# Kernel optimization log

Hardware: AMD Instinct MI355X
Metric: run time of the kernel (lower is better)

## Reference

```python
import jax, jax.numpy as jnp
import numpy as np

B, S, DA, DV, DU, L, M = 16, 256, 1, 32, 1, 4, 12


def conv1x1(x, w, b):
    # x: [B,C,H,W], w: [O,C], b: [O]
    return jnp.einsum('bchw,oc->bohw', x, w) + b[None, :, None, None]


def setup_inputs() -> dict:
    key = jax.random.key(0)
    ks = jax.random.split(key, 12)
    sc = 0.02
    return {
        'x':    jax.random.normal(ks[0], (B, S, S, DA), dtype=jnp.float32),
        'p_w':  sc * jax.random.normal(ks[1], (DV, DA + 2), dtype=jnp.float32),
        'p_b':  sc * jax.random.normal(ks[2], (DV,), dtype=jnp.float32),
        'ws_w': sc * jax.random.normal(ks[3], (L, DV, DV), dtype=jnp.float32),
        'ws_b': sc * jax.random.normal(ks[4], (L, DV), dtype=jnp.float32),
        'w1r':  sc * jax.random.normal(ks[5], (L, DV, DV, M, M), dtype=jnp.float32),
        'w1i':  sc * jax.random.normal(ks[6], (L, DV, DV, M, M), dtype=jnp.float32),
        'w2r':  sc * jax.random.normal(ks[7], (L, DV, DV, M, M), dtype=jnp.float32),
        'w2i':  sc * jax.random.normal(ks[8], (L, DV, DV, M, M), dtype=jnp.float32),
        'q_w':  sc * jax.random.normal(ks[9], (DU, DV), dtype=jnp.float32),
        'q_b':  sc * jax.random.normal(ks[10], (DU,), dtype=jnp.float32),
    }


def fourier_layer(x, w1r, w1i, w2r, w2i):
    # x: [B,C,H,W]; FFT norm None == 'backward' (numpy/jax default)
    b, c, h, w = x.shape
    x_ft = jnp.fft.rfft2(x)                       # [B,C,H,W//2+1] complex
    W1 = w1r + 1j * w1i                           # [C,C,M,M]
    W2 = w2r + 1j * w2i
    top = jnp.einsum('bixy,ioxy->boxy', x_ft[:, :, :M, :M], W1)
    bot = jnp.einsum('bixy,ioxy->boxy', x_ft[:, :, -M:, :M], W2)
    out_ft = jnp.zeros((b, c, h, w // 2 + 1), dtype=x_ft.dtype)
    out_ft = out_ft.at[:, :, :M, :M].set(top)
    out_ft = out_ft.at[:, :, h - M:, :M].set(bot)
    return jnp.fft.irfft2(out_ft, s=(h, w))


def reference(x, p_w, p_b, ws_w, ws_b, w1r, w1i, w2r, w2i, q_w, q_b):
    b, sx, sy, _ = x.shape
    # grid as in get_grid (requires sx == sy, as the original implicitly does)
    gx = jnp.linspace(-1.0, 1.0, sx, dtype=jnp.float32)
    gy = jnp.linspace(-1.0, 1.0, sy, dtype=jnp.float32)
    gridx = jnp.broadcast_to(gx.reshape(1, 1, sx, 1), (b, sy, sx, 1))
    gridy = jnp.broadcast_to(gy.reshape(1, sy, 1, 1), (b, sy, sx, 1))
    grid = jnp.concatenate([gridy, gridx], axis=-1)     # [B,Sy,Sx,2]
    h = jnp.concatenate([x, grid], axis=-1)             # [B,S,S,DA+2]
    h = jnp.transpose(h, (0, 3, 1, 2))                  # NCHW
    h = conv1x1(h, p_w, p_b)                            # lifting
    for i in range(L):
        x1 = fourier_layer(h, w1r[i], w1i[i], w2r[i], w2i[i])
        x2 = conv1x1(h, ws_w[i], ws_b[i])
        h = x1 + x2
        if i < L - 1:
            h = jax.nn.relu(h)
    h = conv1x1(h, q_w, q_b)                            # projection -> [B,1,S,S]
    return jnp.transpose(h, (0, 2, 3, 1)).squeeze(-1)   # [B,S,S]
```

## Files before the change

kernel.cpp:

```cpp
#include <hip/hip_runtime.h>
#include <math.h>

#define NB 16
#define SS 256
#define DV 32
#define MM 12
#define MK 24
#define LL 4
#define TWO_PI_N 0.024543692606170259679f


__global__ __launch_bounds__(256) void k_prep(const float* __restrict__ ws_w,
        float* __restrict__ twT, float* __restrict__ wT)
{
    int j = threadIdx.x;
    #pragma unroll
    for (int k = 0; k < MM; ++k) {
        float ang = TWO_PI_N * (float)((k * j) & 255);
        float s, c; sincosf(ang, &s, &c);
        twT[j * (MM * 2) + 2 * k]     = c;
        twT[j * (MM * 2) + 2 * k + 1] = -s;
    }
    for (int idx = threadIdx.x; idx < LL * DV * DV; idx += 256) {
        int l = idx >> 10, rem = idx & 1023, co = rem >> 5, ci = rem & 31;
        wT[(l * DV + ci) * DV + co] = ws_w[(l * DV + co) * DV + ci];
    }
}

__global__ __launch_bounds__(256) void k_lift(const float* __restrict__ x,
        const float* __restrict__ p_w, const float* __restrict__ p_b,
        float* __restrict__ h)
{
    int tid = threadIdx.x;
    int lane = tid & 63;
    int w = __builtin_amdgcn_readfirstlane(tid >> 6);
    int b  = blockIdx.x >> 6;
    int iy = ((blockIdx.x & 63) << 2) + w;
    int j0 = lane << 2;

    float4 xv = *(const float4*)(x + ((size_t)(b * SS + iy)) * SS + j0);
    float gy = -1.f + 2.f * (float)iy * (1.f / 255.f);
    float4 gx;
    gx.x = -1.f + 2.f * (float)j0 * (1.f / 255.f);
    gx.y = gx.x + 2.f / 255.f; gx.z = gx.y + 2.f / 255.f; gx.w = gx.z + 2.f / 255.f;

    float* hb = h + ((size_t)b * DV * SS + iy) * SS + j0;
    #pragma unroll
    for (int c = 0; c < DV; ++c) {
        float w0 = p_w[3*c], w1 = p_w[3*c+1], w2 = p_w[3*c+2], bb = p_b[c];
        float4 v;
        v.x = w0 * xv.x + w1 * gy + w2 * gx.x + bb;
        v.y = w0 * xv.y + w1 * gy + w2 * gx.y + bb;
        v.z = w0 * xv.z + w1 * gy + w2 * gx.z + bb;
        v.w = w0 * xv.w + w1 * gy + w2 * gx.w + bb;
        *(float4*)(hb + (size_t)c * SS * SS) = v;
    }
}

__global__ __launch_bounds__(512, 4) void k_rowdft(const float* __restrict__ h,
        const float* __restrict__ twT, float* __restrict__ A)
{
    __shared__ float red[MM * 2][SS];
    int tid = threadIdx.x;
    int iy = tid & 255;
    int half = __builtin_amdgcn_readfirstlane(tid >> 8);
    int b = blockIdx.x >> 5, c = blockIdx.x & 31;

    const float4* hr = (const float4*)(h + ((size_t)blockIdx.x * SS + iy) * SS
                                         + half * 128);
    float ar[MM], ai[MM];
    #pragma unroll
    for (int k = 0; k < MM; ++k) { ar[k] = 0.f; ai[k] = 0.f; }

    #pragma unroll 4
    for (int j4 = 0; j4 < 32; ++j4) {
        float4 v = hr[j4];
        float vv[4] = {v.x, v.y, v.z, v.w};
        #pragma unroll
        for (int u = 0; u < 4; ++u) {
            const float* twj = twT + (size_t)(half * 128 + 4 * j4 + u) * (MM * 2);
            float vu = vv[u];
            #pragma unroll
            for (int k = 0; k < 6; ++k) {
                ar[2*k]   += vu * twj[4*k];
                ai[2*k]   += vu * twj[4*k + 1];
                ar[2*k+1] += vu * twj[4*k + 2];
                ai[2*k+1] += vu * twj[4*k + 3];
            }
        }
    }

    if (half == 0) {
        #pragma unroll
        for (int k = 0; k < MM; ++k) {
            red[2*k][iy]     = ar[k];
            red[2*k + 1][iy] = ai[k];
        }
    }
    __syncthreads();
    if (half == 1) {
        #pragma unroll
        for (int ky = 0; ky < MM; ++ky) {
            float2 val;
            val.x = ar[ky] + red[2*ky][iy];
            val.y = ai[ky] + red[2*ky + 1][iy];
            size_t o = ((((size_t)b * MM + ky) * DV + c) * SS + iy) * 2;
            *(float2*)&A[o] = val;
        }
    }
}

__global__ __launch_bounds__(256, 4) void k_coldft(const float* __restrict__ A,
        float* __restrict__ Fin)
{
    int blk = blockIdx.x;
    int mg = blk & 3;
    int bk = blk >> 2;
    int tid = threadIdx.x;
    int c = tid >> 3, ch = tid & 7;
    int iy0 = ch * 32;

    const float2* Ap = (const float2*)(A + ((size_t)bk * DV + c) * SS * 2);

    float fr[6], fi[6], pc[6], ps[6], sc[6], ssn[6];
    #pragma unroll
    for (int k = 0; k < 6; ++k) {
        int m = mg * 6 + k;
        int f = (m < MM) ? m : (232 + m);
        float s, cc;
        sincosf(TWO_PI_N * (float)f, &s, &cc);
        sc[k] = cc; ssn[k] = s;
        sincosf(TWO_PI_N * (float)((f * iy0) & 255), &s, &cc);
        pc[k] = cc; ps[k] = s;
        fr[k] = fi[k] = 0.f;
    }
    #pragma unroll 4
    for (int i = 0; i < 32; ++i) {
        float2 a = Ap[iy0 + i];
        #pragma unroll
        for (int k = 0; k < 6; ++k) {
            fr[k] += a.x * pc[k] + a.y * ps[k];
            fi[k] += a.y * pc[k] - a.x * ps[k];
            float np = pc[k] * sc[k] - ps[k] * ssn[k];
            float nq = pc[k] * ssn[k] + ps[k] * sc[k];
            pc[k] = np; ps[k] = nq;
        }
    }
    #pragma unroll
    for (int m = 1; m < 8; m <<= 1) {
        #pragma unroll
        for (int k = 0; k < 6; ++k) {
            fr[k] += __shfl_xor(fr[k], m, 64);
            fi[k] += __shfl_xor(fi[k], m, 64);
        }
    }
    #pragma unroll
    for (int k = 0; k < 6; ++k) {
        if (ch == k) {
            int m = mg * 6 + k;
            size_t o = (((size_t)bk * DV + c) * MK + m) * 2;
            Fin[o] = fr[k]; Fin[o + 1] = fi[k];
        }
    }
}

__global__ __launch_bounds__(256) void k_mix2(const float* __restrict__ FinG,
        const float* __restrict__ w1r, const float* __restrict__ w1i,
        const float* __restrict__ w2r, const float* __restrict__ w2i,
        float* __restrict__ F, int l)
{
    __shared__ float Fin[DV][MK * 2 + 2];
    int tid = threadIdx.x;
    int b = blockIdx.x / MM, ky = blockIdx.x % MM;

    const float* Fs = FinG + ((size_t)(b * MM + ky)) * DV * MK * 2;
    for (int idx = tid; idx < DV * MK * 2; idx += 256) {
        int c = idx / (MK * 2), r = idx % (MK * 2);
        Fin[c][r] = Fs[idx];
    }
    __syncthreads();

    int o = tid >> 3, set = tid & 7;
    float scale = ((ky == 0) ? 1.0f : 2.0f) * (1.0f / 65536.0f);
    #pragma unroll
    for (int k = 0; k < 3; ++k) {
        int m = set + 8 * k;
        const float* Wr; const float* Wi; int xm;
        if (m < MM) { Wr = w1r; Wi = w1i; xm = m; }
        else        { Wr = w2r; Wi = w2i; xm = m - MM; }
        float orr = 0.f, oii = 0.f;
        for (int i = 0; i < DV; ++i) {
            float gr = Fin[i][2 * m], gi = Fin[i][2 * m + 1];
            size_t wi = ((size_t)(l * DV + i) * DV + o) * (MM * MM) + xm * MM + ky;
            float wr = Wr[wi], wim = Wi[wi];
            orr += gr * wr - gi * wim;
            oii += gr * wim + gi * wr;
        }
        size_t off = ((((size_t)b * MM + ky) * DV + o) * MK + m) * 2;
        F[off] = orr * scale; F[off + 1] = oii * scale;
    }
}

__global__ __launch_bounds__(384) void k_inv1(const float* __restrict__ F,
        float* __restrict__ g)
{
    __shared__ float itw[MK * 2];
    int tid = threadIdx.x;
    int b = blockIdx.x >> 8, iy = blockIdx.x & 255;
    if (tid < MK) {
        int f = (tid < MM) ? tid : (232 + tid);
        float ang = TWO_PI_N * (float)((f * iy) & 255);
        float s, c; sincosf(ang, &s, &c);
        itw[2 * tid] = c; itw[2 * tid + 1] = s;
    }
    __syncthreads();

    int ky = tid >> 5, co = tid & 31;
    const float2* Fp = (const float2*)(F + ((((size_t)b * MM + ky) * DV + co) * MK) * 2);
    float gr = 0.f, gi = 0.f;
    #pragma unroll
    for (int m = 0; m < MK; ++m) {
        float2 fv = Fp[m];
        float ic = itw[2 * m], is = itw[2 * m + 1];
        gr += fv.x * ic - fv.y * is;
        gi += fv.x * is + fv.y * ic;
    }
    size_t o = (((size_t)(b * SS + iy)) * MM + ky) * (DV * 2) + 2 * co;
    g[o] = gr; g[o + 1] = gi;
}

template<int FINAL>
__global__ __launch_bounds__(256, 2) void k_pt(float* __restrict__ h,
        const float* __restrict__ g, const float* __restrict__ wT,
        const float* __restrict__ ws_b, const float* __restrict__ q_w,
        const float* __restrict__ q_b, float* __restrict__ out, int l)
{
    int tid = threadIdx.x;
    int lane = tid & 63;
    int w = __builtin_amdgcn_readfirstlane(tid >> 6);
    int b  = blockIdx.x >> 6;
    int iy = ((blockIdx.x & 63) << 2) + w;
    int j0 = lane << 2;

    float* hb = h + ((size_t)b * DV * SS + iy) * SS + j0;
    const float* wt  = wT + (size_t)l * DV * DV;
    const float* wsb = ws_b + (size_t)l * DV;

    float4 acc[DV];
    #pragma unroll
    for (int co = 0; co < DV; ++co) {
        float bv = wsb[co];
        acc[co].x = bv; acc[co].y = bv; acc[co].z = bv; acc[co].w = bv;
    }

    #pragma unroll 4
    for (int ci = 0; ci < DV; ++ci) {
        float4 hv = *(const float4*)(hb + (size_t)ci * SS * SS);
        const float* wc = wt + ci * DV;
        #pragma unroll
        for (int co = 0; co < DV; ++co) {
            float wv = wc[co];
            acc[co].x += wv * hv.x; acc[co].y += wv * hv.y;
            acc[co].z += wv * hv.z; acc[co].w += wv * hv.w;
        }
    }

    const float* gp = g + ((size_t)(b * SS + iy)) * (MM * DV * 2);
    #pragma unroll 2
    for (int ky = 0; ky < MM; ++ky) {
        float s0, c0, st, ct;
        sincosf(TWO_PI_N * (float)((ky * j0) & 255), &s0, &c0);
        sincosf(TWO_PI_N * (float)ky, &st, &ct);
        float cs[4], sn[4];
        cs[0] = c0; sn[0] = s0;
        #pragma unroll
        for (int u = 1; u < 4; ++u) {
            float nc = cs[u-1] * ct - sn[u-1] * st;
            float ns = sn[u-1] * ct + cs[u-1] * st;
            cs[u] = nc; sn[u] = ns;
        }
        const float* Gk = gp + ky * (DV * 2);
        #pragma unroll
        for (int co = 0; co < DV; ++co) {
            float gr = Gk[2 * co], gi = Gk[2 * co + 1];
            acc[co].x += gr * cs[0] - gi * sn[0];
            acc[co].y += gr * cs[1] - gi * sn[1];
            acc[co].z += gr * cs[2] - gi * sn[2];
            acc[co].w += gr * cs[3] - gi * sn[3];
        }
    }

    if (FINAL) {
        float qb = q_b[0];
        float4 o4; o4.x = qb; o4.y = qb; o4.z = qb; o4.w = qb;
        #pragma unroll
        for (int co = 0; co < DV; ++co) {
            float qv = q_w[co];
            o4.x += qv * acc[co].x; o4.y += qv * acc[co].y;
            o4.z += qv * acc[co].z; o4.w += qv * acc[co].w;
        }
        *(float4*)(out + ((size_t)(b * SS + iy)) * SS + j0) = o4;
    } else {
        #pragma unroll
        for (int co = 0; co < DV; ++co) {
            float4 v;
            v.x = fmaxf(acc[co].x, 0.f); v.y = fmaxf(acc[co].y, 0.f);
            v.z = fmaxf(acc[co].z, 0.f); v.w = fmaxf(acc[co].w, 0.f);
            *(float4*)(hb + (size_t)co * SS * SS) = v;
        }
    }
}

extern "C" void kernel_launch(void* const* d_in, const int* in_sizes, int n_in,
                              void* d_out, int out_size, void* d_ws, size_t ws_size,
                              hipStream_t stream)
{
    const float* x    = (const float*)d_in[0];
    const float* p_w  = (const float*)d_in[1];
    const float* p_b  = (const float*)d_in[2];
    const float* ws_w = (const float*)d_in[3];
    const float* ws_b = (const float*)d_in[4];
    const float* w1r  = (const float*)d_in[5];
    const float* w1i  = (const float*)d_in[6];
    const float* w2r  = (const float*)d_in[7];
    const float* w2i  = (const float*)d_in[8];
    const float* q_w  = (const float*)d_in[9];
    const float* q_b  = (const float*)d_in[10];
    float* out = (float*)d_out;

    float* h   = (float*)d_ws;
    float* A   = h   + (size_t)NB * DV * SS * SS;
    float* F   = A   + (size_t)NB * MM * DV * SS * 2;
    float* g   = F   + (size_t)NB * MM * DV * MK * 2;
    float* Fin = g   + (size_t)NB * SS * MM * DV * 2;
    float* twT = Fin + (size_t)NB * MM * DV * MK * 2;
    float* wT  = twT + (size_t)SS * MM * 2;

    dim3 blk(256);
    k_prep<<<1, blk, 0, stream>>>(ws_w, twT, wT);
    k_lift<<<NB * 64, blk, 0, stream>>>(x, p_w, p_b, h);
    for (int l = 0; l < LL; ++l) {
        k_rowdft<<<NB * DV, dim3(512), 0, stream>>>(h, twT, A);
        k_coldft<<<NB * MM * 4, blk, 0, stream>>>(A, Fin);
        k_mix2<<<NB * MM, blk, 0, stream>>>(Fin, w1r, w1i, w2r, w2i, F, l);
        k_inv1<<<NB * SS, dim3(384), 0, stream>>>(F, g);
        if (l < LL - 1)
            k_pt<0><<<NB * 64, blk, 0, stream>>>(h, g, wT, ws_b,
                                                 nullptr, nullptr, nullptr, l);
        else
            k_pt<1><<<NB * 64, blk, 0, stream>>>(h, g, wT, ws_b,
                                                 q_w, q_b, out, l);
    }
}
```

Measured before the change: 832.0 us.

## Fuse column DFT with spectral mixing; retile pointwise kernel with precomputed twiddles

```diff
diff --git a/kernel.cpp b/kernel.cpp
--- a/kernel.cpp
+++ b/kernel.cpp
@@ -11,7 +11,7 @@
 
 
 __global__ __launch_bounds__(256) void k_prep(const float* __restrict__ ws_w,
-        float* __restrict__ twT, float* __restrict__ wT)
+        float* __restrict__ twT, float* __restrict__ wT, float* __restrict__ tw2)
 {
     int j = threadIdx.x;
     #pragma unroll
@@ -20,6 +20,8 @@
         float s, c; sincosf(ang, &s, &c);
         twT[j * (MM * 2) + 2 * k]     = c;
         twT[j * (MM * 2) + 2 * k + 1] = -s;
+        tw2[(k * SS + j) * 2]     = c;
+        tw2[(k * SS + j) * 2 + 1] = s;
     }
     for (int idx = threadIdx.x; idx < LL * DV * DV; idx += 256) {
         int l = idx >> 10, rem = idx & 1023, co = rem >> 5, ci = rem & 31;
@@ -110,12 +112,16 @@
     }
 }
 
-__global__ __launch_bounds__(256, 4) void k_coldft(const float* __restrict__ A,
-        float* __restrict__ Fin)
-{
+__global__ __launch_bounds__(256, 4) void k_cm(const float* __restrict__ A,
+        const float* __restrict__ w1r, const float* __restrict__ w1i,
+        const float* __restrict__ w2r, const float* __restrict__ w2i,
+        float* __restrict__ F, int l)
+{
+    __shared__ float FinS[DV][6][2];
     int blk = blockIdx.x;
     int mg = blk & 3;
     int bk = blk >> 2;
+    int ky = bk % MM;
     int tid = threadIdx.x;
     int c = tid >> 3, ch = tid & 7;
     int iy0 = ch * 32;
@@ -156,47 +162,27 @@
     }
     #pragma unroll
     for (int k = 0; k < 6; ++k) {
-        if (ch == k) {
-            int m = mg * 6 + k;
-            size_t o = (((size_t)bk * DV + c) * MK + m) * 2;
-            Fin[o] = fr[k]; Fin[o + 1] = fi[k];
-        }
-    }
-}
-
-__global__ __launch_bounds__(256) void k_mix2(const float* __restrict__ FinG,
-        const float* __restrict__ w1r, const float* __restrict__ w1i,
-        const float* __restrict__ w2r, const float* __restrict__ w2i,
-        float* __restrict__ F, int l)
-{
-    __shared__ float Fin[DV][MK * 2 + 2];
-    int tid = threadIdx.x;
-    int b = blockIdx.x / MM, ky = blockIdx.x % MM;
-
-    const float* Fs = FinG + ((size_t)(b * MM + ky)) * DV * MK * 2;
-    for (int idx = tid; idx < DV * MK * 2; idx += 256) {
-        int c = idx / (MK * 2), r = idx % (MK * 2);
-        Fin[c][r] = Fs[idx];
+        if (ch == k) { FinS[c][k][0] = fr[k]; FinS[c][k][1] = fi[k]; }
     }
     __syncthreads();
 
-    int o = tid >> 3, set = tid & 7;
-    float scale = ((ky == 0) ? 1.0f : 2.0f) * (1.0f / 65536.0f);
-    #pragma unroll
-    for (int k = 0; k < 3; ++k) {
-        int m = set + 8 * k;
+    if (ch < 6) {
+        int o = c;
+        int m = mg * 6 + ch;
         const float* Wr; const float* Wi; int xm;
         if (m < MM) { Wr = w1r; Wi = w1i; xm = m; }
         else        { Wr = w2r; Wi = w2i; xm = m - MM; }
+        float scale = ((ky == 0) ? 1.0f : 2.0f) * (1.0f / 65536.0f);
         float orr = 0.f, oii = 0.f;
+        #pragma unroll 4
         for (int i = 0; i < DV; ++i) {
-            float gr = Fin[i][2 * m], gi = Fin[i][2 * m + 1];
+            float gr = FinS[i][ch][0], gi = FinS[i][ch][1];
             size_t wi = ((size_t)(l * DV + i) * DV + o) * (MM * MM) + xm * MM + ky;
             float wr = Wr[wi], wim = Wi[wi];
             orr += gr * wr - gi * wim;
             oii += gr * wim + gi * wr;
         }
-        size_t off = ((((size_t)b * MM + ky) * DV + o) * MK + m) * 2;
+        size_t off = (((size_t)bk * DV + o) * MK + m) * 2;
         F[off] = orr * scale; F[off + 1] = oii * scale;
     }
 }
@@ -230,83 +216,69 @@
 }
 
 template<int FINAL>
-__global__ __launch_bounds__(256, 2) void k_pt(float* __restrict__ h,
+__global__ __launch_bounds__(256, 4) void k_pt(float* __restrict__ h,
         const float* __restrict__ g, const float* __restrict__ wT,
-        const float* __restrict__ ws_b, const float* __restrict__ q_w,
-        const float* __restrict__ q_b, float* __restrict__ out, int l)
+        const float* __restrict__ ws_b, const float* __restrict__ tw2,
+        const float* __restrict__ q_w, const float* __restrict__ q_b,
+        float* __restrict__ out, int l)
 {
     int tid = threadIdx.x;
     int lane = tid & 63;
     int w = __builtin_amdgcn_readfirstlane(tid >> 6);
-    int b  = blockIdx.x >> 6;
-    int iy = ((blockIdx.x & 63) << 2) + w;
-    int j0 = lane << 2;
+    int b  = blockIdx.x >> 7;
+    int iy = ((blockIdx.x & 127) << 1) + (w >> 1);
+    int j0 = ((w & 1) << 7) + (lane << 1);
 
     float* hb = h + ((size_t)b * DV * SS + iy) * SS + j0;
     const float* wt  = wT + (size_t)l * DV * DV;
     const float* wsb = ws_b + (size_t)l * DV;
 
-    float4 acc[DV];
+    float2 acc[DV];
     #pragma unroll
     for (int co = 0; co < DV; ++co) {
         float bv = wsb[co];
-        acc[co].x = bv; acc[co].y = bv; acc[co].z = bv; acc[co].w = bv;
+        acc[co].x = bv; acc[co].y = bv;
     }
 
     #pragma unroll 4
     for (int ci = 0; ci < DV; ++ci) {
-        float4 hv = *(const float4*)(hb + (size_t)ci * SS * SS);
+        float2 hv = *(const float2*)(hb + (size_t)ci * SS * SS);
         const float* wc = wt + ci * DV;
         #pragma unroll
         for (int co = 0; co < DV; ++co) {
             float wv = wc[co];
             acc[co].x += wv * hv.x; acc[co].y += wv * hv.y;
-            acc[co].z += wv * hv.z; acc[co].w += wv * hv.w;
         }
     }
 
     const float* gp = g + ((size_t)(b * SS + iy)) * (MM * DV * 2);
     #pragma unroll 2
     for (int ky = 0; ky < MM; ++ky) {
-        float s0, c0, st, ct;
-        sincosf(TWO_PI_N * (float)((ky * j0) & 255), &s0, &c0);
-        sincosf(TWO_PI_N * (float)ky, &st, &ct);
-        float cs[4], sn[4];
-        cs[0] = c0; sn[0] = s0;
-        #pragma unroll
-        for (int u = 1; u < 4; ++u) {
-            float nc = cs[u-1] * ct - sn[u-1] * st;
-            float ns = sn[u-1] * ct + cs[u-1] * st;
-            cs[u] = nc; sn[u] = ns;
-        }
+        float4 t4 = *(const float4*)(tw2 + ((size_t)ky * SS + j0) * 2);
         const float* Gk = gp + ky * (DV * 2);
         #pragma unroll
         for (int co = 0; co < DV; ++co) {
             float gr = Gk[2 * co], gi = Gk[2 * co + 1];
-            acc[co].x += gr * cs[0] - gi * sn[0];
-            acc[co].y += gr * cs[1] - gi * sn[1];
-            acc[co].z += gr * cs[2] - gi * sn[2];
-            acc[co].w += gr * cs[3] - gi * sn[3];
+            acc[co].x += gr * t4.x - gi * t4.y;
+            acc[co].y += gr * t4.z - gi * t4.w;
         }
     }
 
     if (FINAL) {
         float qb = q_b[0];
-        float4 o4; o4.x = qb; o4.y = qb; o4.z = qb; o4.w = qb;
+        float2 o2; o2.x = qb; o2.y = qb;
         #pragma unroll
         for (int co = 0; co < DV; ++co) {
             float qv = q_w[co];
-            o4.x += qv * acc[co].x; o4.y += qv * acc[co].y;
-            o4.z += qv * acc[co].z; o4.w += qv * acc[co].w;
-        }
-        *(float4*)(out + ((size_t)(b * SS + iy)) * SS + j0) = o4;
+            o2.x += qv * acc[co].x; o2.y += qv * acc[co].y;
+        }
+        *(float2*)(out + ((size_t)(b * SS + iy)) * SS + j0) = o2;
     } else {
         #pragma unroll
         for (int co = 0; co < DV; ++co) {
-            float4 v;
+            float2 v;
             v.x = fmaxf(acc[co].x, 0.f); v.y = fmaxf(acc[co].y, 0.f);
-            v.z = fmaxf(acc[co].z, 0.f); v.w = fmaxf(acc[co].w, 0.f);
-            *(float4*)(hb + (size_t)co * SS * SS) = v;
+            *(float2*)(hb + (size_t)co * SS * SS) = v;
         }
     }
 }
@@ -332,23 +304,22 @@
     float* A   = h   + (size_t)NB * DV * SS * SS;
     float* F   = A   + (size_t)NB * MM * DV * SS * 2;
     float* g   = F   + (size_t)NB * MM * DV * MK * 2;
-    float* Fin = g   + (size_t)NB * SS * MM * DV * 2;
-    float* twT = Fin + (size_t)NB * MM * DV * MK * 2;
+    float* twT = g   + (size_t)NB * SS * MM * DV * 2;
     float* wT  = twT + (size_t)SS * MM * 2;
+    float* tw2 = wT  + (size_t)LL * DV * DV;
 
     dim3 blk(256);
-    k_prep<<<1, blk, 0, stream>>>(ws_w, twT, wT);
+    k_prep<<<1, blk, 0, stream>>>(ws_w, twT, wT, tw2);
     k_lift<<<NB * 64, blk, 0, stream>>>(x, p_w, p_b, h);
     for (int l = 0; l < LL; ++l) {
         k_rowdft<<<NB * DV, dim3(512), 0, stream>>>(h, twT, A);
-        k_coldft<<<NB * MM * 4, blk, 0, stream>>>(A, Fin);
-        k_mix2<<<NB * MM, blk, 0, stream>>>(Fin, w1r, w1i, w2r, w2i, F, l);
+        k_cm<<<NB * MM * 4, blk, 0, stream>>>(A, w1r, w1i, w2r, w2i, F, l);
         k_inv1<<<NB * SS, dim3(384), 0, stream>>>(F, g);
         if (l < LL - 1)
-            k_pt<0><<<NB * 64, blk, 0, stream>>>(h, g, wT, ws_b,
-                                                 nullptr, nullptr, nullptr, l);
+            k_pt<0><<<NB * 128, blk, 0, stream>>>(h, g, wT, ws_b, tw2,
+                                                  nullptr, nullptr, nullptr, l);
         else
-            k_pt<1><<<NB * 64, blk, 0, stream>>>(h, g, wT, ws_b,
-                                                 q_w, q_b, out, l);
-    }
-}
+            k_pt<1><<<NB * 128, blk, 0, stream>>>(h, g, wT, ws_b, tw2,
+                                                  q_w, q_b, out, l);
+    }
+}
```

Measured after the change: 737.5 us. -11.4%, faster.
